# Kernel optimization log

Hardware: AMD Instinct MI355X
Metric: run time of the kernel (lower is better)

The kernel has to match this reference:

```python
import jax, jax.numpy as jnp
import numpy as np
from jax.ops import segment_sum

N_NODES = 100000
IN, HID, OUT = 512, 128, 40
N_EDGES = 1600000


def gcn_conv(x, W, b, src, dst, n):
    # x: [N, d_in] -> linear transform first (PyG GCNConv applies lin before propagate)
    h = x @ W  # [N, d_out]
    # add self-loops
    loop = jnp.arange(n, dtype=src.dtype)
    s = jnp.concatenate([src, loop])
    d = jnp.concatenate([dst, loop])
    # symmetric normalization deg^{-1/2}[s] * deg^{-1/2}[d], deg over targets incl. self-loops
    deg = segment_sum(jnp.ones_like(d, dtype=h.dtype), d, num_segments=n)
    dinv = jnp.where(deg > 0, jax.lax.rsqrt(deg), 0.0)
    norm = dinv[s] * dinv[d]  # [E+N]
    msg = h[s] * norm[:, None]  # gather + scale
    out = segment_sum(msg, d, num_segments=n)  # scatter-add over edges
    return out + b


def setup_inputs() -> dict:
    key = jax.random.key(0)
    k1, k2, k3, k4, k5, k6 = jax.random.split(key, 6)
    x = jax.random.normal(k1, (N_NODES, IN), dtype=jnp.float32)
    edge_index = jax.random.randint(k2, (2, N_EDGES), 0, N_NODES, dtype=jnp.int64)
    s1 = 1.0 / np.sqrt(IN)
    s2 = 1.0 / np.sqrt(HID)
    W1 = jax.random.uniform(k3, (IN, HID), jnp.float32, -s1, s1)
    b1 = jnp.zeros((HID,), jnp.float32)
    W2 = jax.random.uniform(k4, (HID, OUT), jnp.float32, -s2, s2)
    b2 = jnp.zeros((OUT,), jnp.float32)
    return {"x": x, "edge_index": edge_index, "W1": W1, "b1": b1, "W2": W2, "b2": b2}


def reference(x, edge_index, W1, b1, W2, b2):
    src, dst = edge_index[0], edge_index[1]
    n = x.shape[0]
    # CRD: GCNConv -> relu (dropout is identity in eval mode)
    h = jax.nn.relu(gcn_conv(x, W1, b1, src, dst, n))
    # CLS: GCNConv -> log_softmax
    out = gcn_conv(h, W2, b2, src, dst, n)
    return jax.nn.log_softmax(out, axis=1)
```

## Files before the change

kernel.cpp:

```cpp
#include <hip/hip_runtime.h>
#include <hip/hip_bf16.h>

typedef unsigned short u16;
typedef __attribute__((ext_vector_type(8))) short short8;
typedef __attribute__((ext_vector_type(4))) float f32x4;

#define NN   100000
#define NE   1600000
#define DIN  512
#define DHID 128
#define DOUT 40
#define NB   98

__device__ __forceinline__ float bf2f(u16 u) {
  union { unsigned int i; float f; } v; v.i = ((unsigned int)u) << 16; return v.f;
}
__device__ __forceinline__ u16 f2bf(float f) {
  __hip_bfloat16 h = __float2bfloat16(f);
  return *reinterpret_cast<u16*>(&h);
}


__global__ __launch_bounds__(256) void k_count(const int* __restrict__ ei, int* __restrict__ cnt,
                                               int* __restrict__ ticket) {
  int base = (blockIdx.x * 256 + threadIdx.x) * 4;
  if (base >= NE) return;
  int4 d4 = *(const int4*)&ei[NE + base];
  int t0 = atomicAdd(&cnt[d4.x], 1);
  int t1 = atomicAdd(&cnt[d4.y], 1);
  int t2 = atomicAdd(&cnt[d4.z], 1);
  int t3 = atomicAdd(&cnt[d4.w], 1);
  *(int4*)&ticket[base] = make_int4(t0, t1, t2, t3);
}

__global__ __launch_bounds__(256) void k_dinv(const int* __restrict__ cnt, float* __restrict__ dinv) {
  int i = blockIdx.x * 256 + threadIdx.x;
  if (i < NN) dinv[i] = rsqrtf((float)(cnt[i] + 1));
}

__global__ __launch_bounds__(256) void k_blocksum(const int* __restrict__ cnt, int* __restrict__ bsum) {
  __shared__ int s[256];
  int b = blockIdx.x, t = threadIdx.x;
  int base = b * 1024 + t * 4;
  int tot = 0;
  if (base < NN) { int4 v = *(const int4*)&cnt[base]; tot = v.x + v.y + v.z + v.w; }
  s[t] = tot; __syncthreads();
  for (int o = 128; o > 0; o >>= 1) { if (t < o) s[t] += s[t + o]; __syncthreads(); }
  if (t == 0) bsum[b] = s[0];
}

__global__ __launch_bounds__(128) void k_scanbsum(int* __restrict__ bsum) {
  __shared__ int s[128];
  int t = threadIdx.x;
  int v = (t < NB) ? bsum[t] : 0;
  s[t] = v; __syncthreads();
  for (int o = 1; o < 128; o <<= 1) {
    int add = (t >= o) ? s[t - o] : 0;
    __syncthreads();
    s[t] += add;
    __syncthreads();
  }
  if (t < NB) bsum[t] = s[t] - v;
}

__global__ __launch_bounds__(256) void k_scan3(const int* __restrict__ cnt, const int* __restrict__ bsum,
                                               int* __restrict__ offs) {
  __shared__ int s[256];
  int b = blockIdx.x, t = threadIdx.x;
  int base = b * 1024 + t * 4;
  int4 v = make_int4(0, 0, 0, 0);
  if (base < NN) v = *(const int4*)&cnt[base];
  int tot = v.x + v.y + v.z + v.w;
  s[t] = tot; __syncthreads();
  for (int o = 1; o < 256; o <<= 1) {
    int add = (t >= o) ? s[t - o] : 0;
    __syncthreads();
    s[t] += add;
    __syncthreads();
  }
  int tp = s[t] - tot;
  int b0 = bsum[b] + tp;
  if (base < NN) {
    int4 o4;
    o4.x = b0;
    o4.y = b0 + v.x;
    o4.z = b0 + v.x + v.y;
    o4.w = b0 + v.x + v.y + v.z;
    *(int4*)&offs[base] = o4;
  }
  if (b == 0 && t == 0) offs[NN] = NE;
}

__global__ __launch_bounds__(256) void k_scatter(const int* __restrict__ ei, const int* __restrict__ offs,
                                                 const int* __restrict__ ticket, const float* __restrict__ dinv,
                                                 int2* __restrict__ ep) {
  int base = (blockIdx.x * 256 + threadIdx.x) * 4;
  if (base >= NE) return;
  int4 s4 = *(const int4*)&ei[base];
  int4 d4 = *(const int4*)&ei[NE + base];
  int4 t4 = *(const int4*)&ticket[base];
  int p0 = offs[d4.x] + t4.x;
  int p1 = offs[d4.y] + t4.y;
  int p2 = offs[d4.z] + t4.z;
  int p3 = offs[d4.w] + t4.w;
  ep[p0] = make_int2(s4.x, __float_as_int(dinv[s4.x]));
  ep[p1] = make_int2(s4.y, __float_as_int(dinv[s4.y]));
  ep[p2] = make_int2(s4.z, __float_as_int(dinv[s4.z]));
  ep[p3] = make_int2(s4.w, __float_as_int(dinv[s4.w]));
}


__global__ __launch_bounds__(256) void k_prepw(const float* __restrict__ W1, u16* __restrict__ wt) {
  int id = blockIdx.x * 256 + threadIdx.x;
  int k = id & 511, n = id >> 9;
  wt[n * DIN + k] = f2bf(W1[k * DHID + n]);
}


__global__ __launch_bounds__(256) void k_gemm1(const float* __restrict__ x, const u16* __restrict__ wt,
                                               u16* __restrict__ h1) {
  __shared__ u16 xs[64][72];
  __shared__ u16 ws[128][72];
  int t = threadIdx.x;
  int row0 = blockIdx.x * 64;
  int w = t >> 6, l = t & 63;
  int lm = l & 15, lq = l >> 4;
  int mbase = w * 16;
  f32x4 acc[8];
#pragma unroll
  for (int nt = 0; nt < 8; nt++) acc[nt] = (f32x4){0.f, 0.f, 0.f, 0.f};

  for (int c = 0; c < 8; c++) {
    int k0 = c * 64;
#pragma unroll
    for (int it = 0; it < 4; it++) {
      int u = t + it * 256;
      int row = u >> 4, seg = u & 15;
      int gr = row0 + row;
      float4 v = make_float4(0.f, 0.f, 0.f, 0.f);
      if (gr < NN) v = *(const float4*)&x[gr * DIN + k0 + seg * 4];
      ushort4 o;
      o.x = f2bf(v.x); o.y = f2bf(v.y); o.z = f2bf(v.z); o.w = f2bf(v.w);
      *(ushort4*)&xs[row][seg * 4] = o;
    }
#pragma unroll
    for (int it = 0; it < 4; it++) {
      int u = t + it * 256;
      int n = u >> 3, seg = u & 7;
      *(uint4*)&ws[n][seg * 8] = *(const uint4*)&wt[n * DIN + k0 + seg * 8];
    }
    __syncthreads();
#pragma unroll
    for (int s = 0; s < 2; s++) {
      short8 a = *(const short8*)&xs[mbase + lm][s * 32 + lq * 8];
#pragma unroll
      for (int nt = 0; nt < 8; nt++) {
        short8 b = *(const short8*)&ws[nt * 16 + lm][s * 32 + lq * 8];
        acc[nt] = __builtin_amdgcn_mfma_f32_16x16x32_bf16(a, b, acc[nt], 0, 0, 0);
      }
    }
    __syncthreads();
  }
#pragma unroll
  for (int reg = 0; reg < 4; reg++) {
    int gr = row0 + mbase + lq * 4 + reg;
    if (gr < NN) {
#pragma unroll
      for (int nt = 0; nt < 8; nt++) {
        h1[gr * DHID + nt * 16 + lm] = f2bf(acc[nt][reg]);
      }
    }
  }
}


__global__ __launch_bounds__(256) void k_prop1(const u16* __restrict__ h1, const float* __restrict__ dinv,
                                               const int* __restrict__ offs, const int2* __restrict__ ep,
                                               const float* __restrict__ b1, u16* __restrict__ g) {
  int n = blockIdx.x * 4 + (threadIdx.x >> 6);
  int l = threadIdx.x & 63;
  int qtr = l >> 4, c = l & 15;
  int fb = c * 8;
  float dn = dinv[n];
  float a[8];
#pragma unroll
  for (int j = 0; j < 8; j++) a[j] = 0.f;
  if (qtr == 0) {
    short8 sv = *(const short8*)&h1[n * DHID + fb];
#pragma unroll
    for (int j = 0; j < 8; j++) a[j] = dn * bf2f((u16)sv[j]);
  }
  int e1 = offs[n + 1];
  int q = offs[n] + qtr * 4;
  for (; q + 3 < e1; q += 16) {
    int2 ea = ep[q], eb = ep[q + 1], ec = ep[q + 2], ed = ep[q + 3];
    float wa = __int_as_float(ea.y), wb = __int_as_float(eb.y);
    float wc = __int_as_float(ec.y), wd = __int_as_float(ed.y);
    short8 va = *(const short8*)&h1[ea.x * DHID + fb];
    short8 vb = *(const short8*)&h1[eb.x * DHID + fb];
    short8 vc = *(const short8*)&h1[ec.x * DHID + fb];
    short8 vd = *(const short8*)&h1[ed.x * DHID + fb];
#pragma unroll
    for (int j = 0; j < 8; j++)
      a[j] += wa * bf2f((u16)va[j]) + wb * bf2f((u16)vb[j])
            + wc * bf2f((u16)vc[j]) + wd * bf2f((u16)vd[j]);
  }
  for (; q < e1; q++) {
    int2 ea = ep[q];
    float wa = __int_as_float(ea.y);
    short8 va = *(const short8*)&h1[ea.x * DHID + fb];
#pragma unroll
    for (int j = 0; j < 8; j++) a[j] += wa * bf2f((u16)va[j]);
  }
#pragma unroll
  for (int j = 0; j < 8; j++) {
    a[j] += __shfl_xor(a[j], 16);
    a[j] += __shfl_xor(a[j], 32);
  }
  if (qtr == 0) {
    float4 b0 = *(const float4*)&b1[fb];
    float4 b4 = *(const float4*)&b1[fb + 4];
    float bb[8] = {b0.x, b0.y, b0.z, b0.w, b4.x, b4.y, b4.z, b4.w};
    short8 o;
#pragma unroll
    for (int j = 0; j < 8; j++) o[j] = (short)f2bf(fmaxf(bb[j] + dn * a[j], 0.f));
    *(short8*)&g[n * DHID + fb] = o;
  }
}


__global__ __launch_bounds__(320) void k_gemm2(const u16* __restrict__ g, const float* __restrict__ W2,
                                               u16* __restrict__ h2) {
  __shared__ float w2s[DHID][DOUT];
  __shared__ float gs[8][DHID];
  int t = threadIdx.x;
  int row0 = blockIdx.x * 8;
  for (int idx = t; idx < DHID * DOUT; idx += 320) ((float*)w2s)[idx] = W2[idx];
  for (int idx = t; idx < 8 * DHID; idx += 320) {
    int r = idx >> 7, k = idx & 127;
    int gr = row0 + r;
    ((float*)gs)[idx] = (gr < NN) ? bf2f(g[gr * DHID + k]) : 0.f;
  }
  __syncthreads();
  int r = t / DOUT, c = t % DOUT;
  float acc = 0.f;
#pragma unroll
  for (int k = 0; k < DHID; k += 4) {
    float4 gv = *(const float4*)&gs[r][k];
    acc += gv.x * w2s[k][c] + gv.y * w2s[k + 1][c] + gv.z * w2s[k + 2][c] + gv.w * w2s[k + 3][c];
  }
  int gr = row0 + r;
  if (gr < NN) h2[gr * DOUT + c] = f2bf(acc);
}


__global__ __launch_bounds__(256) void k_prop2(const u16* __restrict__ h2, const float* __restrict__ dinv,
                                               const int* __restrict__ offs, const int2* __restrict__ ep,
                                               const float* __restrict__ b2, float* __restrict__ out) {
  int n = blockIdx.x * 4 + (threadIdx.x >> 6);
  int l = threadIdx.x & 63;
  int grp = l >> 5;
  int c2 = l & 31;
  bool act = c2 < 20;
  int f = c2 * 2;
  float dn = dinv[n];
  float a0 = 0.f, a1 = 0.f;
  if (grp == 0 && act) {
    uint sv = *(const uint*)&h2[n * DOUT + f];
    a0 = dn * bf2f((u16)(sv & 0xffffu));
    a1 = dn * bf2f((u16)(sv >> 16));
  }
  int e1 = offs[n + 1];
  int q = offs[n] + grp * 4;
  for (; q + 3 < e1; q += 8) {
    int2 ea = ep[q], eb = ep[q + 1], ec = ep[q + 2], ed = ep[q + 3];
    uint va = act ? *(const uint*)&h2[ea.x * DOUT + f] : 0u;
    uint vb = act ? *(const uint*)&h2[eb.x * DOUT + f] : 0u;
    uint vc = act ? *(const uint*)&h2[ec.x * DOUT + f] : 0u;
    uint vd = act ? *(const uint*)&h2[ed.x * DOUT + f] : 0u;
    float wa = __int_as_float(ea.y), wb = __int_as_float(eb.y);
    float wc = __int_as_float(ec.y), wd = __int_as_float(ed.y);
    a0 += wa * bf2f((u16)(va & 0xffffu)) + wb * bf2f((u16)(vb & 0xffffu))
        + wc * bf2f((u16)(vc & 0xffffu)) + wd * bf2f((u16)(vd & 0xffffu));
    a1 += wa * bf2f((u16)(va >> 16)) + wb * bf2f((u16)(vb >> 16))
        + wc * bf2f((u16)(vc >> 16)) + wd * bf2f((u16)(vd >> 16));
  }
  for (; q < e1; q++) {
    int2 ea = ep[q];
    uint va = act ? *(const uint*)&h2[ea.x * DOUT + f] : 0u;
    float wa = __int_as_float(ea.y);
    a0 += wa * bf2f((u16)(va & 0xffffu));
    a1 += wa * bf2f((u16)(va >> 16));
  }
  a0 += __shfl_xor(a0, 32);
  a1 += __shfl_xor(a1, 32);
  float l0 = act ? (b2[f]     + dn * a0) : -INFINITY;
  float l1 = act ? (b2[f + 1] + dn * a1) : -INFINITY;
  float mx = fmaxf(l0, l1);
#pragma unroll
  for (int o = 16; o > 0; o >>= 1) mx = fmaxf(mx, __shfl_xor(mx, o));
  float pv = act ? (__expf(l0 - mx) + __expf(l1 - mx)) : 0.f;
#pragma unroll
  for (int o = 16; o > 0; o >>= 1) pv += __shfl_xor(pv, o);
  if (grp == 0 && act) {
    float ls = logf(pv);
    *(float2*)&out[n * DOUT + f] = make_float2(l0 - mx - ls, l1 - mx - ls);
  }
}


extern "C" void kernel_launch(void* const* d_in, const int* in_sizes, int n_in,
                              void* d_out, int out_size, void* d_ws, size_t ws_size,
                              hipStream_t stream) {
  const float* x  = (const float*)d_in[0];
  const int* ei   = (const int*)d_in[1];
  const float* W1 = (const float*)d_in[2];
  const float* b1 = (const float*)d_in[3];
  const float* W2 = (const float*)d_in[4];
  const float* b2 = (const float*)d_in[5];
  float* out      = (float*)d_out;

  char* ws = (char*)d_ws;
  int*   cnt    = (int*)(ws + 0);
  float* dinv   = (float*)(ws + 400000);
  int*   offs   = (int*)(ws + 800000);
  int*   bsum   = (int*)(ws + 1200128);
  int2*  ep     = (int2*)(ws + 1200640);
  int*   ticket = (int*)(ws + 14000640);
  u16*   h1     = (u16*)(ws + 20400640);
  u16*   h2     = (u16*)(ws + 20400640);
  u16*   g      = (u16*)(ws + 46000640);
  u16*   wt     = (u16*)(ws + 71600640);

  hipMemsetAsync(cnt, 0, 400000, stream);

  k_count   <<<(NE / 4 + 255) / 256, 256, 0, stream>>>(ei, cnt, ticket);
  k_dinv    <<<(NN + 255) / 256, 256, 0, stream>>>(cnt, dinv);
  k_blocksum<<<NB, 256, 0, stream>>>(cnt, bsum);
  k_scanbsum<<<1, 128, 0, stream>>>(bsum);
  k_scan3   <<<NB, 256, 0, stream>>>(cnt, bsum, offs);
  k_scatter <<<(NE / 4 + 255) / 256, 256, 0, stream>>>(ei, offs, ticket, dinv, ep);

  k_prepw   <<<(DIN * DHID) / 256, 256, 0, stream>>>(W1, wt);
  k_gemm1   <<<(NN + 63) / 64, 256, 0, stream>>>(x, wt, h1);
  k_prop1   <<<NN / 4, 256, 0, stream>>>(h1, dinv, offs, ep, b1, g);
  k_gemm2   <<<(NN + 7) / 8, 320, 0, stream>>>(g, W2, h2);
  k_prop2   <<<NN / 4, 256, 0, stream>>>(h2, dinv, offs, ep, b2, out);
}
```

Before: 672.0 us.

## Double-buffer gemm1 with register prefetch and use atomic cursors for CSR scatter

The layer-1 GEMM now prefetches global tiles two k-chunks ahead into registers and ping-pongs between two LDS buffers, so each chunk needs one barrier and global loads overlap the MFMA work. Separately, the CSR build drops the per-edge ticket array: k_count no longer stores the atomic return values, and k_scatter claims slots with atomics on a cursor copy of the offsets. This removes the ticket write and read traffic but makes edge order within a row nondeterministic, and it adds register and LDS pressure in the GEMM.

After: 734.0 us. 1.09x slower.

```diff
diff --git a/kernel.cpp b/kernel.cpp
--- a/kernel.cpp
+++ b/kernel.cpp
@@ -21,16 +21,14 @@
 }
 
 
-__global__ __launch_bounds__(256) void k_count(const int* __restrict__ ei, int* __restrict__ cnt,
-                                               int* __restrict__ ticket) {
+__global__ __launch_bounds__(256) void k_count(const int* __restrict__ ei, int* __restrict__ cnt) {
   int base = (blockIdx.x * 256 + threadIdx.x) * 4;
   if (base >= NE) return;
   int4 d4 = *(const int4*)&ei[NE + base];
-  int t0 = atomicAdd(&cnt[d4.x], 1);
-  int t1 = atomicAdd(&cnt[d4.y], 1);
-  int t2 = atomicAdd(&cnt[d4.z], 1);
-  int t3 = atomicAdd(&cnt[d4.w], 1);
-  *(int4*)&ticket[base] = make_int4(t0, t1, t2, t3);
+  atomicAdd(&cnt[d4.x], 1);
+  atomicAdd(&cnt[d4.y], 1);
+  atomicAdd(&cnt[d4.z], 1);
+  atomicAdd(&cnt[d4.w], 1);
 }
 
 __global__ __launch_bounds__(256) void k_dinv(const int* __restrict__ cnt, float* __restrict__ dinv) {
@@ -64,7 +62,7 @@
 }
 
 __global__ __launch_bounds__(256) void k_scan3(const int* __restrict__ cnt, const int* __restrict__ bsum,
-                                               int* __restrict__ offs) {
+                                               int* __restrict__ offs, int* __restrict__ cur) {
   __shared__ int s[256];
   int b = blockIdx.x, t = threadIdx.x;
   int base = b * 1024 + t * 4;
@@ -87,22 +85,21 @@
     o4.z = b0 + v.x + v.y;
     o4.w = b0 + v.x + v.y + v.z;
     *(int4*)&offs[base] = o4;
+    *(int4*)&cur[base]  = o4;
   }
   if (b == 0 && t == 0) offs[NN] = NE;
 }
 
-__global__ __launch_bounds__(256) void k_scatter(const int* __restrict__ ei, const int* __restrict__ offs,
-                                                 const int* __restrict__ ticket, const float* __restrict__ dinv,
-                                                 int2* __restrict__ ep) {
+__global__ __launch_bounds__(256) void k_scatter(const int* __restrict__ ei, int* __restrict__ cur,
+                                                 const float* __restrict__ dinv, int2* __restrict__ ep) {
   int base = (blockIdx.x * 256 + threadIdx.x) * 4;
   if (base >= NE) return;
   int4 s4 = *(const int4*)&ei[base];
   int4 d4 = *(const int4*)&ei[NE + base];
-  int4 t4 = *(const int4*)&ticket[base];
-  int p0 = offs[d4.x] + t4.x;
-  int p1 = offs[d4.y] + t4.y;
-  int p2 = offs[d4.z] + t4.z;
-  int p3 = offs[d4.w] + t4.w;
+  int p0 = atomicAdd(&cur[d4.x], 1);
+  int p1 = atomicAdd(&cur[d4.y], 1);
+  int p2 = atomicAdd(&cur[d4.z], 1);
+  int p3 = atomicAdd(&cur[d4.w], 1);
   ep[p0] = make_int2(s4.x, __float_as_int(dinv[s4.x]));
   ep[p1] = make_int2(s4.y, __float_as_int(dinv[s4.y]));
   ep[p2] = make_int2(s4.z, __float_as_int(dinv[s4.z]));
@@ -117,50 +114,69 @@
 }
 
 
+#define G1_LOAD(S, C) do { int k0_ = (C) * 64;                                          \
+  _Pragma("unroll") for (int it = 0; it < 4; it++) {                                    \
+    int u_ = t + it * 256; int row_ = u_ >> 4, seg_ = u_ & 15; int gr_ = row0 + row_;   \
+    xv[S][it] = (gr_ < NN) ? *(const float4*)&x[gr_ * DIN + k0_ + seg_ * 4]             \
+                           : make_float4(0.f, 0.f, 0.f, 0.f);                           \
+    wv[S][it] = *(const uint4*)&wt[(u_ >> 3) * DIN + k0_ + (u_ & 7) * 8];               \
+  } } while (0)
+
+#define G1_WRITE(S) do {                                                                \
+  _Pragma("unroll") for (int it = 0; it < 4; it++) {                                    \
+    int u_ = t + it * 256; int row_ = u_ >> 4, seg_ = u_ & 15;                          \
+    float4 v_ = xv[S][it]; ushort4 o_;                                                  \
+    o_.x = f2bf(v_.x); o_.y = f2bf(v_.y); o_.z = f2bf(v_.z); o_.w = f2bf(v_.w);         \
+    *(ushort4*)&xs[S][row_][seg_ * 4] = o_;                                             \
+    *(uint4*)&ws[S][u_ >> 3][(u_ & 7) * 8] = wv[S][it];                                 \
+  } } while (0)
+
+#define G1_MFMA(S) do {                                                                 \
+  _Pragma("unroll") for (int s2 = 0; s2 < 2; s2++) {                                    \
+    short8 a_ = *(const short8*)&xs[S][mbase + lm][s2 * 32 + lq * 8];                   \
+    _Pragma("unroll") for (int nt = 0; nt < 8; nt++) {                                  \
+      short8 b_ = *(const short8*)&ws[S][nt * 16 + lm][s2 * 32 + lq * 8];               \
+      acc[nt] = __builtin_amdgcn_mfma_f32_16x16x32_bf16(a_, b_, acc[nt], 0, 0, 0);      \
+    } } } while (0)
+
+#define G1_BAR() do {                                                                   \
+    asm volatile("s_waitcnt lgkmcnt(0)" ::: "memory");                                  \
+    __builtin_amdgcn_sched_barrier(0);          \
+    __builtin_amdgcn_s_barrier();                                                       \
+  } while (0)
+
 __global__ __launch_bounds__(256) void k_gemm1(const float* __restrict__ x, const u16* __restrict__ wt,
                                                u16* __restrict__ h1) {
-  __shared__ u16 xs[64][72];
-  __shared__ u16 ws[128][72];
+  __shared__ u16 xs[2][64][72];
+  __shared__ u16 ws[2][128][72];
   int t = threadIdx.x;
   int row0 = blockIdx.x * 64;
   int w = t >> 6, l = t & 63;
   int lm = l & 15, lq = l >> 4;
   int mbase = w * 16;
+  float4 xv[2][4];
+  uint4  wv[2][4];
   f32x4 acc[8];
 #pragma unroll
   for (int nt = 0; nt < 8; nt++) acc[nt] = (f32x4){0.f, 0.f, 0.f, 0.f};
 
+  G1_LOAD(0, 0);
+  G1_LOAD(1, 1);
+  G1_WRITE(0);
+  G1_BAR();
+
+#pragma unroll
   for (int c = 0; c < 8; c++) {
-    int k0 = c * 64;
-#pragma unroll
-    for (int it = 0; it < 4; it++) {
-      int u = t + it * 256;
-      int row = u >> 4, seg = u & 15;
-      int gr = row0 + row;
-      float4 v = make_float4(0.f, 0.f, 0.f, 0.f);
-      if (gr < NN) v = *(const float4*)&x[gr * DIN + k0 + seg * 4];
-      ushort4 o;
-      o.x = f2bf(v.x); o.y = f2bf(v.y); o.z = f2bf(v.z); o.w = f2bf(v.w);
-      *(ushort4*)&xs[row][seg * 4] = o;
+    if (c + 2 < 8) {
+      if ((c & 1) == 0) G1_LOAD(0, c + 2); else G1_LOAD(1, c + 2);
     }
-#pragma unroll
-    for (int it = 0; it < 4; it++) {
-      int u = t + it * 256;
-      int n = u >> 3, seg = u & 7;
-      *(uint4*)&ws[n][seg * 8] = *(const uint4*)&wt[n * DIN + k0 + seg * 8];
+    if ((c & 1) == 0) G1_MFMA(0); else G1_MFMA(1);
+    if (c + 1 < 8) {
+      if ((c & 1) == 0) G1_WRITE(1); else G1_WRITE(0);
+      G1_BAR();
     }
-    __syncthreads();
-#pragma unroll
-    for (int s = 0; s < 2; s++) {
-      short8 a = *(const short8*)&xs[mbase + lm][s * 32 + lq * 8];
-#pragma unroll
-      for (int nt = 0; nt < 8; nt++) {
-        short8 b = *(const short8*)&ws[nt * 16 + lm][s * 32 + lq * 8];
-        acc[nt] = __builtin_amdgcn_mfma_f32_16x16x32_bf16(a, b, acc[nt], 0, 0, 0);
-      }
-    }
-    __syncthreads();
-  }
+  }
+
 #pragma unroll
   for (int reg = 0; reg < 4; reg++) {
     int gr = row0 + mbase + lq * 4 + reg;
@@ -326,7 +342,7 @@
   int*   offs   = (int*)(ws + 800000);
   int*   bsum   = (int*)(ws + 1200128);
   int2*  ep     = (int2*)(ws + 1200640);
-  int*   ticket = (int*)(ws + 14000640);
+  int*   cur    = (int*)(ws + 14000640);
   u16*   h1     = (u16*)(ws + 20400640);
   u16*   h2     = (u16*)(ws + 20400640);
   u16*   g      = (u16*)(ws + 46000640);
@@ -334,12 +350,12 @@
 
   hipMemsetAsync(cnt, 0, 400000, stream);
 
-  k_count   <<<(NE / 4 + 255) / 256, 256, 0, stream>>>(ei, cnt, ticket);
+  k_count   <<<(NE / 4 + 255) / 256, 256, 0, stream>>>(ei, cnt);
   k_dinv    <<<(NN + 255) / 256, 256, 0, stream>>>(cnt, dinv);
   k_blocksum<<<NB, 256, 0, stream>>>(cnt, bsum);
   k_scanbsum<<<1, 128, 0, stream>>>(bsum);
-  k_scan3   <<<NB, 256, 0, stream>>>(cnt, bsum, offs);
-  k_scatter <<<(NE / 4 + 255) / 256, 256, 0, stream>>>(ei, offs, ticket, dinv, ep);
+  k_scan3   <<<NB, 256, 0, stream>>>(cnt, bsum, offs, cur);
+  k_scatter <<<(NE / 4 + 255) / 256, 256, 0, stream>>>(ei, cur, dinv, ep);
 
   k_prepw   <<<(DIN * DHID) / 256, 256, 0, stream>>>(W1, wt);
   k_gemm1   <<<(NN + 63) / 64, 256, 0, stream>>>(x, wt, h1);
```
